# Kernel tuning notes

Measured on AMD Instinct MI355X. Metric: run time of the kernel, lower is better.

## Reference

```python
import jax, jax.numpy as jnp
import numpy as np

B, P, C = 32, 8732, 21
TOP_K = 200
CONF_THRESH = 0.01
NMS_THRESH = 0.45
VAR0, VAR1 = 0.1, 0.2  # VOC PRIOR_BOX VARIANCE


def setup_inputs() -> dict:
    key = jax.random.key(0)
    k1, k2, k3 = jax.random.split(key, 3)
    loc_data = jax.random.normal(k1, (B, P, 4), jnp.float32)
    conf_data = jax.random.uniform(k2, (B, P, C), jnp.float32)
    prior_data = jax.random.uniform(k3, (P, 4), jnp.float32)
    return {"loc_data": loc_data, "conf_data": conf_data, "prior_data": prior_data}


def _decode(loc, priors):
    # priors are (cx, cy, w, h); returns (x1, y1, x2, y2)
    cxcy = priors[:, :2] + loc[:, :2] * VAR0 * priors[:, 2:]
    wh = priors[:, 2:] * jnp.exp(loc[:, 2:] * VAR1)
    x1y1 = cxcy - wh * 0.5
    return jnp.concatenate([x1y1, x1y1 + wh], axis=1)  # [P,4]


def _nms_class(boxes, scores):
    # boxes [P,4], scores [P] -> [TOP_K,5] rows of (score, x1, y1, x2, y2)
    s = jnp.where(scores > CONF_THRESH, scores, -1.0)
    top_s, idx = jax.lax.top_k(s, TOP_K)          # descending scores
    b = boxes[idx]                                 # [K,4]
    valid = top_s > CONF_THRESH
    x1, y1, x2, y2 = b[:, 0], b[:, 1], b[:, 2], b[:, 3]
    area = (x2 - x1) * (y2 - y1)
    # pairwise intersection / IoU [K,K]
    xx1 = jnp.maximum(x1[:, None], x1[None, :])
    yy1 = jnp.maximum(y1[:, None], y1[None, :])
    xx2 = jnp.minimum(x2[:, None], x2[None, :])
    yy2 = jnp.minimum(y2[:, None], y2[None, :])
    inter = jnp.clip(xx2 - xx1, 0.0) * jnp.clip(yy2 - yy1, 0.0)
    union = area[:, None] + area[None, :] - inter
    iou = inter / union
    ar = jnp.arange(TOP_K)

    def step(carry, j):
        kept, suppressed = carry
        is_kept = valid[j] & ~suppressed[j]
        kept = kept.at[j].set(is_kept)
        suppressed = suppressed | (is_kept & (iou[j] > NMS_THRESH) & (ar > j))
        return (kept, suppressed), None

    (kept, _), _ = jax.lax.scan(
        step, (jnp.zeros(TOP_K, bool), jnp.zeros(TOP_K, bool)), ar)
    # compact kept rows to the front (matches output[i, cl, :count] = ...)
    pos = jnp.cumsum(kept) - 1
    safe = jnp.where(kept, pos, TOP_K)
    rows = jnp.concatenate([top_s[:, None], b], axis=1)  # [K,5]
    out = jnp.zeros((TOP_K + 1, 5), rows.dtype).at[safe].set(rows)[:TOP_K]
    return out


def reference(loc_data, conf_data, prior_data):
    def per_image(loc, conf):
        boxes = _decode(loc, prior_data)           # [P,4]
        return jax.vmap(lambda s: _nms_class(boxes, s), in_axes=1)(conf)  # [C,K,5]

    out = jax.vmap(per_image)(loc_data, conf_data)  # [B,C,K,5]
    return out.at[:, 0].set(0.0)  # class 0 (background) is skipped in original
```

## Files before the change

kernel.cpp:

```cpp
#include <hip/hip_runtime.h>
#include <stdint.h>

#define B_ 32
#define P_ 8732
#define C_ 21
#define TOPK 200
#define TGT 228
#define TGT0 245
#define SUBCAP 28
#define NCH2 35
#define NSLOT (NCH2 * SUBCAP)
#define CONF_T 0.01f
#define NMS_T 0.45f
#define NT 512
#define KV4 5
#define NTASK (B_ * C_)

__device__ __forceinline__ uint32_t f2s(float f) {
    uint32_t u = __float_as_uint(f);
    return (u & 0x80000000u) ? ~u : (u | 0x80000000u);
}
__device__ __forceinline__ float s2f(uint32_t s) {
    uint32_t b = (s & 0x80000000u) ? (s & 0x7FFFFFFFu) : ~s;
    return __uint_as_float(b);
}
__device__ __forceinline__ uint32_t keyof(float v) {
    return f2s((v > CONF_T) ? v : -1.0f);
}
__device__ __forceinline__ uint32_t thr0() {
    return f2s(1.0f - (float)TGT0 / (float)P_);
}

__global__ __launch_bounds__(256) void scatter_cands(const float* __restrict__ conf,
                                                     uint32_t* __restrict__ gccnt,
                                                     uint64_t* __restrict__ gcand) {
    const int b = blockIdx.x / NCH2;
    const int ch = blockIdx.x % NCH2;
    const int p0 = ch * 256;
    const int n = min(256, P_ - p0);
    const int tid = threadIdx.x;
    const int lane = tid & 63;
    const int wv = tid >> 6;
    __shared__ float tile[256 * C_];
    const float4* src4 = (const float4*)(conf + ((size_t)b * P_ + p0) * C_);
    float4* tile4 = (float4*)tile;
    const int tot4 = (n * C_) >> 2;
    for (int i = tid; i < tot4; i += 256) tile4[i] = src4[i];
    __syncthreads();
    const uint32_t T0 = thr0();
    const unsigned long long lmask = (1ull << lane) - 1ull;
    for (int c = (wv == 0 ? 4 : wv); c < C_; c += 4) {
        int base = 0;
        uint64_t* dst = gcand + ((size_t)(b * C_ + c) * NCH2 + ch) * SUBCAP;
        #pragma unroll
        for (int itp = 0; itp < 4; ++itp) {
            const int p = itp * 64 + lane;
            bool q = false; uint32_t key = 0;
            if (p < n) {
                key = keyof(tile[p * C_ + c]);
                q = (key >= T0);
            }
            const unsigned long long bm = __ballot(q);
            if (q) {
                int pos = base + (int)__popcll(bm & lmask);
                if (pos < SUBCAP)
                    dst[pos] = ((uint64_t)key << 32) | (uint32_t)(~(uint32_t)(p0 + p));
            }
            base += (int)__popcll(bm);
        }
        if (lane == 0) gccnt[(size_t)(b * C_ + c) * NCH2 + ch] = (uint32_t)base;
    }
}

template<bool HASWS>
__global__ __launch_bounds__(NT, 6) void detect_kernel(
    const float* __restrict__ loc, const float* __restrict__ prior,
    const uint32_t* __restrict__ gccnt, const uint64_t* __restrict__ gcand,
    const float* __restrict__ conf, float* __restrict__ out)
{
    const int task = blockIdx.x;
    const int b = task / C_;
    const int c = task % C_;
    const int tid = threadIdx.x;
    const int lane = tid & 63;
    float* outp = out + (size_t)task * TOPK * 5;

    if (c == 0) {
        for (int e = tid; e < TOPK * 5; e += NT) outp[e] = 0.0f;
        return;
    }

    __shared__ uint64_t cand[256];
    __shared__ float4 bbox[TOPK];
    __shared__ float bs[TOPK];
    __shared__ unsigned long long msk[TOPK * 4];
    __shared__ unsigned long long vmask[4];
    __shared__ int order[TOPK];
    __shared__ int s_cnt, s_nk;
    __shared__ int s_c2[2];
    __shared__ uint32_t s_ccnt[NCH2];
    __shared__ int s_gc, s_bad;

    const uint32_t T0 = thr0();

    uint64_t vc0 = 0, vc1 = 0;
    if (HASWS) {
        const uint64_t* gp = gcand + (size_t)task * NSLOT;
        vc0 = gp[tid];
        if (tid + NT < NSLOT) vc1 = gp[tid + NT];
        if (tid < NCH2) s_ccnt[tid] = gccnt[(size_t)task * NCH2 + tid];
    }

    if (tid == 0) s_cnt = 0;
    if (tid < 2) s_c2[tid] = 0;
    for (int i2 = tid; i2 < TOPK * 4; i2 += NT) msk[i2] = 0ull;
    __syncthreads();
    if (HASWS && tid < 64) {
        uint32_t cc = (lane < NCH2) ? s_ccnt[lane] : 0u;
        int bad = (cc > SUBCAP) ? 1 : 0;
        int tot = (int)cc;
        #pragma unroll
        for (int d = 1; d < 64; d <<= 1) {
            tot += __shfl_down(tot, d);
            bad |= __shfl_down(bad, d);
        }
        if (lane == 0) { s_gc = tot; s_bad = bad; }
    }
    __syncthreads();

    const bool fast = HASWS && !s_bad && s_gc >= TOPK;
    const int gc = HASWS ? s_gc : 0;

    bool val0 = false, val1 = false;
    uint4 kv[KV4];
    if (fast) {
        {
            const int ch0 = tid / SUBCAP, i0 = tid - ch0 * SUBCAP;
            val0 = i0 < (int)s_ccnt[ch0];
        }
        const int s1 = tid + NT;
        if (s1 < NSLOT) {
            const int ch1 = s1 / SUBCAP, i1 = s1 - ch1 * SUBCAP;
            val1 = i1 < (int)s_ccnt[ch1];
        }
    } else {
        const float* sp = conf + (size_t)b * P_ * C_ + c;
        #pragma unroll
        for (int r = 0; r < KV4; ++r) {
            uint32_t uu[4];
            #pragma unroll
            for (int c4 = 0; c4 < 4; ++c4) {
                int p = (tid + r * NT) * 4 + c4;
                if (p < P_) {
                    float v = sp[(size_t)p * C_];
                    v = (v > CONF_T) ? v : -1.0f;
                    uu[c4] = f2s(v);
                } else uu[c4] = 0u;
            }
            kv[r] = make_uint4(uu[0], uu[1], uu[2], uu[3]);
        }
    }

    if (fast) {
        uint32_t vthr = T0;
        if (gc > 256) {
            const uint32_t k0 = (uint32_t)(vc0 >> 32);
            const uint32_t k1 = (uint32_t)(vc1 >> 32);
            uint32_t lo = T0, hi = 0xFFFFFFFFu;
            uint32_t t;
            {
                const float sc = s2f(T0);
                const float sn = 1.0f - (1.0f - sc) * (float)TGT / (float)gc;
                t = f2s(sn);
                if (!(t > lo && t < hi)) t = lo + ((hi - lo) >> 1);
            }
            for (int it = 0; ; ++it) {
                const int slot = it & 1;
                int my = (val0 && k0 >= t) + (val1 && k1 >= t);
                #pragma unroll
                for (int d = 1; d < 64; d <<= 1) my += __shfl_down(my, d);
                if (lane == 0) atomicAdd(&s_c2[slot], my);
                __syncthreads();
                const int cnt = s_c2[slot];
                __syncthreads();
                if (tid == 0) s_c2[slot] = 0;
                if (cnt >= TOPK && cnt <= 256) { vthr = t; break; }
                if (cnt > 256) lo = t; else hi = t;
                if (hi - lo <= 1) { vthr = lo; break; }
                uint32_t tn = 0;
                bool bis = (it >= 8) || (cnt == 0);
                if (!bis) {
                    const float sc = s2f(t);
                    const float sn = 1.0f - (1.0f - sc) * (float)TGT / (float)cnt;
                    tn = f2s(sn);
                    if (!(tn > lo && tn < hi)) bis = true;
                }
                if (bis) tn = lo + ((hi - lo) >> 1);
                t = tn;
            }
        }
        if (val0 && (uint32_t)(vc0 >> 32) >= vthr) {
            int pos = atomicAdd(&s_cnt, 1);
            if (pos < 256) cand[pos] = vc0;
        }
        if (val1 && (uint32_t)(vc1 >> 32) >= vthr) {
            int pos = atomicAdd(&s_cnt, 1);
            if (pos < 256) cand[pos] = vc1;
        }
    } else {
        uint32_t lo = 0u, hi = 0xFFFFFFFFu;
        uint32_t t = f2s(1.0f - (float)TGT / (float)P_);
        uint32_t vthr = 0u;
        for (int it = 0; ; ++it) {
            const int slot = it & 1;
            int my = 0;
            #pragma unroll
            for (int r = 0; r < KV4; ++r)
                my += (kv[r].x >= t) + (kv[r].y >= t) + (kv[r].z >= t) + (kv[r].w >= t);
            #pragma unroll
            for (int d = 1; d < 64; d <<= 1) my += __shfl_down(my, d);
            if (lane == 0) atomicAdd(&s_c2[slot], my);
            __syncthreads();
            const int cnt = s_c2[slot];
            __syncthreads();
            if (tid == 0) s_c2[slot] = 0;
            if (cnt >= TOPK && cnt <= 256) { vthr = t; break; }
            if (cnt > 256) lo = t; else hi = t;
            if (hi - lo <= 1) { vthr = lo; break; }
            uint32_t tn = 0;
            bool bis = (it >= 8) || (cnt == 0);
            if (!bis) {
                const float sc = s2f(t);
                const float sn = 1.0f - (1.0f - sc) * (float)TGT / (float)cnt;
                tn = f2s(sn);
                if (!(tn > lo && tn < hi)) bis = true;
            }
            if (bis) tn = lo + ((hi - lo) >> 1);
            t = tn;
        }
        #pragma unroll
        for (int r = 0; r < KV4; ++r) {
            const int pb = (tid + r * NT) * 4;
            uint32_t uu[4] = {kv[r].x, kv[r].y, kv[r].z, kv[r].w};
            #pragma unroll
            for (int c4 = 0; c4 < 4; ++c4) {
                uint32_t u = uu[c4];
                if (u >= vthr) {
                    int pos = atomicAdd(&s_cnt, 1);
                    if (pos < 256) cand[pos] = ((uint64_t)u << 32) | (uint32_t)(~(uint32_t)(pb + c4));
                }
            }
        }
    }
    __syncthreads();
    if (tid < 256 && tid >= s_cnt) cand[tid] = 0ull;
    __syncthreads();

    uint64_t v = (tid < 256) ? cand[tid] : 0ull;
    for (int kk = 2; kk <= 256; kk <<= 1) {
        for (int j = kk >> 1; j > 0; j >>= 1) {
            if (j >= 64) {
                __syncthreads();
                if (tid < 256) cand[tid] = v;
                __syncthreads();
                if (tid < 256) {
                    uint64_t pv = cand[tid ^ j];
                    bool keepmax = (((tid & j) == 0) == ((tid & kk) == 0));
                    v = keepmax ? (v > pv ? v : pv) : (v < pv ? v : pv);
                }
            } else if (tid < 256) {
                uint64_t pv = __shfl_xor(v, j);
                bool keepmax = (((tid & j) == 0) == ((tid & kk) == 0));
                v = keepmax ? (v > pv ? v : pv) : (v < pv ? v : pv);
            }
        }
    }

    float my_sc = -1.0f;
    if (tid < TOPK) {
        uint32_t su = (uint32_t)(v >> 32);
        int p = (int)(~(uint32_t)v);
        my_sc = s2f(su);
        const float4 l4 = *(const float4*)(loc + ((size_t)b * P_ + p) * 4);
        const float4 pr = *(const float4*)(prior + (size_t)p * 4);
        float cx = __fadd_rn(pr.x, __fmul_rn(__fmul_rn(l4.x, 0.1f), pr.z));
        float cy = __fadd_rn(pr.y, __fmul_rn(__fmul_rn(l4.y, 0.1f), pr.w));
        float ew = (float)exp((double)__fmul_rn(l4.z, 0.2f));
        float eh = (float)exp((double)__fmul_rn(l4.w, 0.2f));
        float w  = __fmul_rn(pr.z, ew);
        float h  = __fmul_rn(pr.w, eh);
        float x1 = __fsub_rn(cx, __fmul_rn(w, 0.5f));
        float y1 = __fsub_rn(cy, __fmul_rn(h, 0.5f));
        float x2 = __fadd_rn(x1, w);
        float y2 = __fadd_rn(y1, h);
        bs[tid] = my_sc;
        bbox[tid] = make_float4(x1, y1, x2, y2);
    }
    {
        unsigned long long bm = __ballot(tid < TOPK && my_sc > CONF_T);
        if (lane == 0 && tid < 256) vmask[tid >> 6] = bm;
    }
    __syncthreads();

    if (tid < 500) {
        const int rp = tid / 5;
        const int s  = tid - rp * 5;
        #pragma unroll
        for (int pass = 0; pass < 2; ++pass) {
            const int j  = pass ? (199 - rp) : rp;
            const int i0 = j + 1 + s;
            const float4 bj = bbox[j];
            const float  aj = __fmul_rn(__fsub_rn(bj.z, bj.x), __fsub_rn(bj.w, bj.y));
            for (int i = i0; i < TOPK; i += 5) {
                const float4 bi = bbox[i];
                float xx1 = fmaxf(bj.x, bi.x);
                float yy1 = fmaxf(bj.y, bi.y);
                float xx2 = fminf(bj.z, bi.z);
                float yy2 = fminf(bj.w, bi.w);
                float dx = fmaxf(__fsub_rn(xx2, xx1), 0.0f);
                float dy = fmaxf(__fsub_rn(yy2, yy1), 0.0f);
                float inter = __fmul_rn(dx, dy);
                if (inter > 0.0f) {
                    float ai = __fmul_rn(__fsub_rn(bi.z, bi.x), __fsub_rn(bi.w, bi.y));
                    float uni = __fsub_rn(__fadd_rn(aj, ai), inter);
                    float t45 = __fmul_rn(NMS_T, uni);
                    float mar = __fmul_rn(t45, 1e-6f);
                    bool sup;
                    if (inter > __fadd_rn(t45, mar)) sup = true;
                    else if (inter < __fsub_rn(t45, mar)) sup = false;
                    else sup = (inter / uni > NMS_T);
                    if (sup) atomicOr(&msk[j * 4 + (i >> 6)], 1ull << (i & 63));
                }
            }
        }
    }
    __syncthreads();

    if (tid < 64) {
        const int L = tid;
        auto or_reduce = [&](unsigned long long x) {
            #pragma unroll
            for (int d = 1; d < 64; d <<= 1) x |= __shfl_xor(x, d);
            return x;
        };
        unsigned long long s1 = 0, s2 = 0, s3 = 0;
        int nk = 0;
        #pragma unroll
        for (int w = 0; w < 4; ++w) {
            const int j = (w << 6) | L;
            unsigned long long r0 = 0, r1 = 0, r2 = 0, r3 = 0;
            if (j < TOPK) {
                const unsigned long long* mr = &msk[j * 4];
                r0 = mr[0]; r1 = mr[1]; r2 = mr[2]; r3 = mr[3];
            }
            const unsigned long long rself = (w == 0) ? r0 : (w == 1) ? r1
                                           : (w == 2) ? r2 : r3;
            unsigned long long sw = (w == 0) ? 0ull : (w == 1) ? s1
                                  : (w == 2) ? s2 : s3;
            unsigned long long alive = vmask[w] & ~sw;
            unsigned long long pm = 0;
            while (alive) {
                int jl = __ffsll(alive) - 1;
                if (L == 0) order[nk] = (w << 6) | jl;
                ++nk;
                sw |= __shfl(rself, jl);
                pm |= (1ull << jl);
                alive &= ~(sw | (1ull << jl));
            }
            if (pm) {
                const bool picked = (pm >> L) & 1ull;
                if (w == 0) {
                    s1 |= or_reduce(picked ? r1 : 0ull);
                    s2 |= or_reduce(picked ? r2 : 0ull);
                    s3 |= or_reduce(picked ? r3 : 0ull);
                } else if (w == 1) {
                    s2 |= or_reduce(picked ? r2 : 0ull);
                    s3 |= or_reduce(picked ? r3 : 0ull);
                } else if (w == 2) {
                    s3 |= or_reduce(picked ? r3 : 0ull);
                }
            }
        }
        if (L == 0) s_nk = nk;
    }
    __syncthreads();

    const int nk = s_nk;
    for (int e = tid; e < TOPK * 5; e += NT) {
        int r = e / 5;
        int f = e - r * 5;
        float val = 0.0f;
        if (r < nk) {
            int j = order[r];
            float4 bb = bbox[j];
            val = (f == 0) ? bs[j] : (f == 1) ? bb.x : (f == 2) ? bb.y
                : (f == 3) ? bb.z : bb.w;
        }
        outp[e] = val;
    }
}

extern "C" void kernel_launch(void* const* d_in, const int* in_sizes, int n_in,
                              void* d_out, int out_size, void* d_ws, size_t ws_size,
                              hipStream_t stream) {
    const float* loc   = (const float*)d_in[0];
    const float* conf  = (const float*)d_in[1];
    const float* prior = (const float*)d_in[2];
    float* out = (float*)d_out;

    const size_t cnt_bytes  = (size_t)NTASK * NCH2 * sizeof(uint32_t);
    const size_t cand_bytes = (size_t)NTASK * NSLOT * sizeof(uint64_t);
    if (ws_size >= cnt_bytes + cand_bytes) {
        uint32_t* gccnt = (uint32_t*)d_ws;
        uint64_t* gcand = (uint64_t*)((char*)d_ws + cnt_bytes);
        scatter_cands<<<B_ * NCH2, 256, 0, stream>>>(conf, gccnt, gcand);
        detect_kernel<true><<<NTASK, NT, 0, stream>>>(loc, prior, gccnt, gcand, conf, out);
    } else {
        detect_kernel<false><<<NTASK, NT, 0, stream>>>(loc, prior, nullptr, nullptr, conf, out);
    }
}
```

Before: 123.7 us.

## Fuse candidate scatter into detect kernel with per-task arrival counters

```diff
diff --git a/kernel.cpp b/kernel.cpp
--- a/kernel.cpp
+++ b/kernel.cpp
@@ -10,6 +10,7 @@
 #define SUBCAP 28
 #define NCH2 35
 #define NSLOT (NCH2 * SUBCAP)
+#define NJOB (B_ * NCH2)
 #define CONF_T 0.01f
 #define NMS_T 0.45f
 #define NT 512
@@ -31,91 +32,111 @@
     return f2s(1.0f - (float)TGT0 / (float)P_);
 }
 
-__global__ __launch_bounds__(256) void scatter_cands(const float* __restrict__ conf,
-                                                     uint32_t* __restrict__ gccnt,
-                                                     uint64_t* __restrict__ gcand) {
-    const int b = blockIdx.x / NCH2;
-    const int ch = blockIdx.x % NCH2;
-    const int p0 = ch * 256;
-    const int n = min(256, P_ - p0);
-    const int tid = threadIdx.x;
-    const int lane = tid & 63;
-    const int wv = tid >> 6;
-    __shared__ float tile[256 * C_];
-    const float4* src4 = (const float4*)(conf + ((size_t)b * P_ + p0) * C_);
-    float4* tile4 = (float4*)tile;
-    const int tot4 = (n * C_) >> 2;
-    for (int i = tid; i < tot4; i += 256) tile4[i] = src4[i];
-    __syncthreads();
-    const uint32_t T0 = thr0();
-    const unsigned long long lmask = (1ull << lane) - 1ull;
-    for (int c = (wv == 0 ? 4 : wv); c < C_; c += 4) {
-        int base = 0;
-        uint64_t* dst = gcand + ((size_t)(b * C_ + c) * NCH2 + ch) * SUBCAP;
-        #pragma unroll
-        for (int itp = 0; itp < 4; ++itp) {
-            const int p = itp * 64 + lane;
-            bool q = false; uint32_t key = 0;
-            if (p < n) {
-                key = keyof(tile[p * C_ + c]);
-                q = (key >= T0);
-            }
-            const unsigned long long bm = __ballot(q);
-            if (q) {
-                int pos = base + (int)__popcll(bm & lmask);
-                if (pos < SUBCAP)
-                    dst[pos] = ((uint64_t)key << 32) | (uint32_t)(~(uint32_t)(p0 + p));
-            }
-            base += (int)__popcll(bm);
-        }
-        if (lane == 0) gccnt[(size_t)(b * C_ + c) * NCH2 + ch] = (uint32_t)base;
-    }
-}
-
 template<bool HASWS>
-__global__ __launch_bounds__(NT, 6) void detect_kernel(
+__global__ __launch_bounds__(NT, 6) void fused_kernel(
     const float* __restrict__ loc, const float* __restrict__ prior,
-    const uint32_t* __restrict__ gccnt, const uint64_t* __restrict__ gcand,
-    const float* __restrict__ conf, float* __restrict__ out)
+    const float* __restrict__ conf,
+    uint32_t* __restrict__ arrive, uint32_t* __restrict__ gccnt,
+    uint64_t* __restrict__ gcand, float* __restrict__ out)
 {
-    const int task = blockIdx.x;
+    const int bid = blockIdx.x;
+    const int task = bid;
     const int b = task / C_;
     const int c = task % C_;
     const int tid = threadIdx.x;
     const int lane = tid & 63;
+    const int wv = tid >> 6;
     float* outp = out + (size_t)task * TOPK * 5;
 
-    if (c == 0) {
-        for (int e = tid; e < TOPK * 5; e += NT) outp[e] = 0.0f;
-        return;
-    }
-
+    __shared__ float tile[256 * C_];
     __shared__ uint64_t cand[256];
     __shared__ float4 bbox[TOPK];
     __shared__ float bs[TOPK];
     __shared__ unsigned long long msk[TOPK * 4];
     __shared__ unsigned long long vmask[4];
     __shared__ int order[TOPK];
-    __shared__ int s_cnt, s_nk;
+    __shared__ int s_cnt, s_nk, s_ok;
     __shared__ int s_c2[2];
     __shared__ uint32_t s_ccnt[NCH2];
     __shared__ int s_gc, s_bad;
 
     const uint32_t T0 = thr0();
 
+    if (HASWS) {
+        const unsigned long long lmask = (1ull << lane) - 1ull;
+        for (int j = bid; j < NJOB; j += NTASK) {
+            const int jb = j / NCH2;
+            const int ch = j - jb * NCH2;
+            const int p0 = ch * 256;
+            const int n = min(256, P_ - p0);
+            const float4* src4 = (const float4*)(conf + ((size_t)jb * P_ + p0) * C_);
+            float4* tile4 = (float4*)tile;
+            const int tot4 = (n * C_) >> 2;
+            for (int i = tid; i < tot4; i += NT) tile4[i] = src4[i];
+            __syncthreads();
+            for (int cc = wv + 1; cc < C_; cc += 8) {
+                int base = 0;
+                uint64_t* dst = gcand + ((size_t)(jb * C_ + cc) * NCH2 + ch) * SUBCAP;
+                #pragma unroll
+                for (int itp = 0; itp < 4; ++itp) {
+                    const int p = itp * 64 + lane;
+                    bool q = false; uint32_t key = 0;
+                    if (p < n) {
+                        key = keyof(tile[p * C_ + cc]);
+                        q = (key >= T0);
+                    }
+                    const unsigned long long bm = __ballot(q);
+                    if (q) {
+                        int pos = base + (int)__popcll(bm & lmask);
+                        if (pos < SUBCAP)
+                            dst[pos] = ((uint64_t)key << 32) | (uint32_t)(~(uint32_t)(p0 + p));
+                    }
+                    base += (int)__popcll(bm);
+                }
+                if (lane == 0) gccnt[(size_t)(jb * C_ + cc) * NCH2 + ch] = (uint32_t)base;
+            }
+            __threadfence();
+            __syncthreads();
+            if (tid >= 1 && tid < C_)
+                __hip_atomic_fetch_add(&arrive[jb * C_ + tid], 1u,
+                                       __ATOMIC_RELEASE, __HIP_MEMORY_SCOPE_AGENT);
+            __syncthreads();
+        }
+    }
+
+    if (c == 0) {
+        for (int e = tid; e < TOPK * 5; e += NT) outp[e] = 0.0f;
+        return;
+    }
+
+    bool wsok = HASWS;
+    if (HASWS) {
+        if (tid == 0) {
+            uint32_t a = 0;
+            for (int it = 0; it < (1 << 22); ++it) {
+                a = __hip_atomic_load(&arrive[task], __ATOMIC_ACQUIRE,
+                                      __HIP_MEMORY_SCOPE_AGENT);
+                if (a >= NCH2) break;
+                __builtin_amdgcn_s_sleep(8);
+            }
+            s_ok = (a >= NCH2);
+        }
+        __syncthreads();
+        wsok = (s_ok != 0);
+    }
+
+    if (tid == 0) s_cnt = 0;
+    if (tid < 2) s_c2[tid] = 0;
+    for (int i2 = tid; i2 < TOPK * 4; i2 += NT) msk[i2] = 0ull;
     uint64_t vc0 = 0, vc1 = 0;
-    if (HASWS) {
+    if (wsok) {
         const uint64_t* gp = gcand + (size_t)task * NSLOT;
         vc0 = gp[tid];
         if (tid + NT < NSLOT) vc1 = gp[tid + NT];
         if (tid < NCH2) s_ccnt[tid] = gccnt[(size_t)task * NCH2 + tid];
     }
-
-    if (tid == 0) s_cnt = 0;
-    if (tid < 2) s_c2[tid] = 0;
-    for (int i2 = tid; i2 < TOPK * 4; i2 += NT) msk[i2] = 0ull;
-    __syncthreads();
-    if (HASWS && tid < 64) {
+    __syncthreads();
+    if (wsok && tid < 64) {
         uint32_t cc = (lane < NCH2) ? s_ccnt[lane] : 0u;
         int bad = (cc > SUBCAP) ? 1 : 0;
         int tot = (int)cc;
@@ -128,8 +149,8 @@
     }
     __syncthreads();
 
-    const bool fast = HASWS && !s_bad && s_gc >= TOPK;
-    const int gc = HASWS ? s_gc : 0;
+    const bool fast = wsok && !s_bad && s_gc >= TOPK;
+    const int gc = wsok ? s_gc : 0;
 
     bool val0 = false, val1 = false;
     uint4 kv[KV4];
@@ -408,14 +429,18 @@
     const float* prior = (const float*)d_in[2];
     float* out = (float*)d_out;
 
+    const size_t arr_bytes  = 4096;
     const size_t cnt_bytes  = (size_t)NTASK * NCH2 * sizeof(uint32_t);
     const size_t cand_bytes = (size_t)NTASK * NSLOT * sizeof(uint64_t);
-    if (ws_size >= cnt_bytes + cand_bytes) {
-        uint32_t* gccnt = (uint32_t*)d_ws;
-        uint64_t* gcand = (uint64_t*)((char*)d_ws + cnt_bytes);
-        scatter_cands<<<B_ * NCH2, 256, 0, stream>>>(conf, gccnt, gcand);
-        detect_kernel<true><<<NTASK, NT, 0, stream>>>(loc, prior, gccnt, gcand, conf, out);
+    if (ws_size >= arr_bytes + cnt_bytes + cand_bytes) {
+        uint32_t* arrive = (uint32_t*)d_ws;
+        uint32_t* gccnt  = (uint32_t*)((char*)d_ws + arr_bytes);
+        uint64_t* gcand  = (uint64_t*)((char*)d_ws + arr_bytes + cnt_bytes);
+        hipMemsetAsync(arrive, 0, (size_t)NTASK * sizeof(uint32_t), stream);
+        fused_kernel<true><<<NTASK, NT, 0, stream>>>(loc, prior, conf,
+                                                     arrive, gccnt, gcand, out);
     } else {
-        detect_kernel<false><<<NTASK, NT, 0, stream>>>(loc, prior, nullptr, nullptr, conf, out);
-    }
-}
+        fused_kernel<false><<<NTASK, NT, 0, stream>>>(loc, prior, conf,
+                                                      nullptr, nullptr, nullptr, out);
+    }
+}
```

Result: slower. 354.6 us (+186.6%).
